# Kernel optimization log

Measured on AMD Instinct MI355X. Metric: run time of the kernel, lower is better.

The kernel has to match this reference:

```python
import jax, jax.numpy as jnp
import numpy as np

B, S, H = 32, 2048, 1024


def setup_inputs() -> dict:
    key = jax.random.key(0)
    k1, k2, k3, k4, k5, k6 = jax.random.split(key, 6)
    sc = 1.0 / np.sqrt(H)
    return {
        "dec_state": jax.random.normal(k1, (B, 1, H), dtype=jnp.float32),
        "enc_state": jax.random.normal(k2, (B, S, 2 * H), dtype=jnp.float32),
        "src_length": jax.random.randint(k3, (B,), 1, S + 1, dtype=jnp.int32),
        "W_enc": jax.random.normal(k4, (H, 2 * H), dtype=jnp.float32) * sc,
        "W_dec": jax.random.normal(k5, (H, H), dtype=jnp.float32) * sc,
        "W_energy": jax.random.normal(k6, (1, H), dtype=jnp.float32) * sc,
    }


def reference(dec_state, enc_state, src_length, W_enc, W_dec, W_energy):
    # enc: [B,S,H], dec: [B,1,H]
    enc = jnp.einsum('bse,he->bsh', enc_state, W_enc)
    dec = jnp.einsum('bod,hd->boh', dec_state, W_dec)
    # energies: [B,S] -> [B,1,S]
    energies = jnp.einsum('bsh,oh->bso', jnp.tanh(dec + enc), W_energy)[..., 0]
    mask = jnp.arange(S)[None, :] < src_length[:, None]  # [B,S]
    energies = jnp.where(mask, energies, -jnp.inf)[:, None, :]  # [B,1,S]
    alphas = jax.nn.softmax(energies, axis=-1)
    context = jnp.einsum('bos,se->boe', alphas[:, 0:1, :].squeeze(1)[:, None, :].squeeze(1)[:, None, :].squeeze(1)[:, None, :], enc_state) if False else jnp.matmul(alphas, enc_state)  # [B,1,2H]
    return context, alphas
```

## Files before the change

kernel.cpp:

```cpp
#include <hip/hip_runtime.h>
#include <hip/hip_bf16.h>
#include <stdint.h>

#define B_  32
#define S_  2048
#define H_  1024
#define K_  2048
#define M_  65536

#define BM  128
#define BN  128
#define BK  32
#define LDK 40

typedef __bf16 bf16x8 __attribute__((ext_vector_type(8)));
typedef float  f32x4  __attribute__((ext_vector_type(4)));

__device__ __forceinline__ unsigned short f2bf(float x) {
    unsigned u = __builtin_bit_cast(unsigned, x);
    u += 0x7fffu + ((u >> 16) & 1u);
    return (unsigned short)(u >> 16);
}

__device__ __forceinline__ float tanh_fast(float x) {
    float e = __expf(2.0f * x);
    return 1.0f - 2.0f / (e + 1.0f);
}

__global__ __launch_bounds__(256) void cast_k(const float* __restrict__ in,
                                              unsigned short* __restrict__ o, int n4) {
    int i = blockIdx.x * 256 + threadIdx.x;
    if (i < n4) {
        float4 v = *(const float4*)(in + (long)i * 4);
        unsigned short h0 = f2bf(v.x), h1 = f2bf(v.y), h2 = f2bf(v.z), h3 = f2bf(v.w);
        uint2 pk;
        pk.x = (unsigned)h0 | ((unsigned)h1 << 16);
        pk.y = (unsigned)h2 | ((unsigned)h3 << 16);
        *(uint2*)(o + (long)i * 4) = pk;
    }
}

__global__ __launch_bounds__(256) void dec_k(const float* __restrict__ ds,
                                             const float* __restrict__ Wd,
                                             float* __restrict__ decv) {
    const int b = blockIdx.y;
    const int w = threadIdx.x >> 6, lane = threadIdx.x & 63;
    const int h = blockIdx.x * 4 + w;
    const float* wr = Wd + (long)h * H_;
    const float* dr = ds + (long)b * H_;
    float acc = 0.f;
#pragma unroll
    for (int i = 0; i < 4; i++) {
        int idx = lane * 4 + i * 256;
        float4 a = *(const float4*)(wr + idx);
        float4 d = *(const float4*)(dr + idx);
        acc += a.x * d.x + a.y * d.y + a.z * d.z + a.w * d.w;
    }
    for (int m2 = 1; m2 < 64; m2 <<= 1) acc += __shfl_xor(acc, m2, 64);
    if (lane == 0) decv[(long)b * H_ + h] = acc;
}

__global__ __launch_bounds__(256) void gemm_energy(const float* __restrict__ A,
                                                   const unsigned short* __restrict__ Bw,
                                                   const float* __restrict__ decv,
                                                   const float* __restrict__ Weng,
                                                   float* __restrict__ pe) {
    __shared__ __align__(16) unsigned short Asm[BM * LDK];
    __shared__ __align__(16) unsigned short Bsm[BN * LDK];
    __shared__ float esum[2][BM];

    const int nb = blockIdx.x, mb = blockIdx.y;
    const int t = threadIdx.x;
    const int lane = t & 63, w = t >> 6;
    const int wm = w >> 1, wn = w & 1;
    const int r = lane & 15, g = lane >> 4;

    f32x4 acc[4][4];
#pragma unroll
    for (int mi = 0; mi < 4; mi++)
#pragma unroll
        for (int ni = 0; ni < 4; ni++)
#pragma unroll
            for (int k = 0; k < 4; k++) acc[mi][ni][k] = 0.f;

    const float* Abase = A + (long)mb * BM * K_;
    const unsigned short* Bbase = Bw + (long)nb * BN * K_;

    for (int kt = 0; kt < K_; kt += BK) {
        __syncthreads();
#pragma unroll
        for (int i = 0; i < 4; i++) {
            int f = t + 256 * i;
            int row = f >> 3, c4 = (f & 7) << 2;
            float4 v = *(const float4*)(Abase + (long)row * K_ + kt + c4);
            unsigned short h0 = f2bf(v.x), h1 = f2bf(v.y), h2 = f2bf(v.z), h3 = f2bf(v.w);
            uint2 pk;
            pk.x = (unsigned)h0 | ((unsigned)h1 << 16);
            pk.y = (unsigned)h2 | ((unsigned)h3 << 16);
            *(uint2*)&Asm[row * LDK + c4] = pk;
        }
#pragma unroll
        for (int j = 0; j < 2; j++) {
            int u = t + 256 * j;
            int row = u >> 2, c8 = (u & 3) << 3;
            uint4 v = *(const uint4*)(Bbase + (long)row * K_ + kt + c8);
            *(uint4*)&Bsm[row * LDK + c8] = v;
        }
        __syncthreads();
        bf16x8 af[4], bfr[4];
#pragma unroll
        for (int mi = 0; mi < 4; mi++)
            af[mi] = *(const bf16x8*)&Asm[(wm * 64 + mi * 16 + r) * LDK + g * 8];
#pragma unroll
        for (int ni = 0; ni < 4; ni++)
            bfr[ni] = *(const bf16x8*)&Bsm[(wn * 64 + ni * 16 + r) * LDK + g * 8];
#pragma unroll
        for (int mi = 0; mi < 4; mi++)
#pragma unroll
            for (int ni = 0; ni < 4; ni++)
                acc[mi][ni] = __builtin_amdgcn_mfma_f32_16x16x32_bf16(af[mi], bfr[ni],
                                                                     acc[mi][ni], 0, 0, 0);
    }

    const int b = mb >> 4;
    float wv[4], dv[4];
#pragma unroll
    for (int ni = 0; ni < 4; ni++) {
        int h = nb * BN + wn * 64 + ni * 16 + r;
        wv[ni] = Weng[h];
        dv[ni] = decv[b * H_ + h];
    }
    float rs[4][4];
#pragma unroll
    for (int mi = 0; mi < 4; mi++)
#pragma unroll
        for (int rr = 0; rr < 4; rr++) rs[mi][rr] = 0.f;
#pragma unroll
    for (int mi = 0; mi < 4; mi++)
#pragma unroll
        for (int ni = 0; ni < 4; ni++)
#pragma unroll
            for (int rr = 0; rr < 4; rr++)
                rs[mi][rr] += wv[ni] * tanh_fast(dv[ni] + acc[mi][ni][rr]);
#pragma unroll
    for (int m2 = 1; m2 < 16; m2 <<= 1)
#pragma unroll
        for (int mi = 0; mi < 4; mi++)
#pragma unroll
            for (int rr = 0; rr < 4; rr++)
                rs[mi][rr] += __shfl_xor(rs[mi][rr], m2, 64);
    if (r == 0) {
#pragma unroll
        for (int mi = 0; mi < 4; mi++)
#pragma unroll
            for (int rr = 0; rr < 4; rr++)
                esum[wn][wm * 64 + mi * 16 + g * 4 + rr] = rs[mi][rr];
    }
    __syncthreads();
    if (t < BM) pe[(long)nb * M_ + (long)mb * BM + t] = esum[0][t] + esum[1][t];
}

__global__ __launch_bounds__(256) void softmax_k(const float* __restrict__ pe,
                                                 const int* __restrict__ slen,
                                                 float* __restrict__ alph) {
    const int b = blockIdx.x, t = threadIdx.x;
    const int len = slen[b];
    __shared__ float sh[4];
    const float NEG = -__builtin_inff();
    float e[8];
    float mx = NEG;
#pragma unroll
    for (int i = 0; i < 8; i++) {
        int s = t + i * 256;
        float v = 0.f;
#pragma unroll
        for (int p = 0; p < 8; p++) v += pe[(long)p * M_ + b * S_ + s];
        v = (s < len) ? v : NEG;
        e[i] = v;
        mx = fmaxf(mx, v);
    }
    for (int m2 = 1; m2 < 64; m2 <<= 1) mx = fmaxf(mx, __shfl_xor(mx, m2, 64));
    if ((t & 63) == 0) sh[t >> 6] = mx;
    __syncthreads();
    mx = fmaxf(fmaxf(sh[0], sh[1]), fmaxf(sh[2], sh[3]));
    float sum = 0.f;
#pragma unroll
    for (int i = 0; i < 8; i++) {
        float x = (e[i] == NEG) ? 0.f : __expf(e[i] - mx);
        e[i] = x;
        sum += x;
    }
    for (int m2 = 1; m2 < 64; m2 <<= 1) sum += __shfl_xor(sum, m2, 64);
    __syncthreads();
    if ((t & 63) == 0) sh[t >> 6] = sum;
    __syncthreads();
    sum = sh[0] + sh[1] + sh[2] + sh[3];
    float inv = 1.0f / sum;
#pragma unroll
    for (int i = 0; i < 8; i++) alph[b * S_ + t + i * 256] = e[i] * inv;
}

__global__ __launch_bounds__(256) void context_k(const float* __restrict__ enc,
                                                 const float* __restrict__ alph,
                                                 const int* __restrict__ slen,
                                                 float* __restrict__ out) {
    const int b = blockIdx.y;
    const int x = blockIdx.x;
    const int ec = x & 1, sc = x >> 1;
    const int len = slen[b];
    const int s0 = sc * 256;
    if (s0 >= len) return;
    const int send = min(s0 + 256, len);
    __shared__ float al[256];
    const int t = threadIdx.x;
    al[t] = alph[b * S_ + s0 + t];
    __syncthreads();
    const int e0 = ec * 1024 + t * 4;
    float ax = 0.f, ay = 0.f, az = 0.f, aw = 0.f;
    const float* base = enc + ((long)b * S_ + s0) * K_ + e0;
#pragma unroll 4
    for (int s = s0; s < send; ++s) {
        float a = al[s - s0];
        float4 v = *(const float4*)base;
        ax += a * v.x; ay += a * v.y; az += a * v.z; aw += a * v.w;
        base += K_;
    }
    float* o = out + (long)b * K_ + e0;
    atomicAdd(o + 0, ax);
    atomicAdd(o + 1, ay);
    atomicAdd(o + 2, az);
    atomicAdd(o + 3, aw);
}

extern "C" void kernel_launch(void* const* d_in, const int* in_sizes, int n_in,
                              void* d_out, int out_size, void* d_ws, size_t ws_size,
                              hipStream_t stream) {
    const float* dec_state = (const float*)d_in[0];
    const float* enc_state = (const float*)d_in[1];
    const int*   src_len   = (const int*)d_in[2];
    const float* W_enc     = (const float*)d_in[3];
    const float* W_dec     = (const float*)d_in[4];
    const float* W_energy  = (const float*)d_in[5];
    float* out = (float*)d_out;

    char* ws = (char*)d_ws;
    float* decv = (float*)ws;
    float* pe   = (float*)(ws + 131072);
    unsigned short* Wenc_bf = (unsigned short*)(ws + 131072 + 2097152);
    float* alph = out + 65536;

    hipMemsetAsync(out, 0, 65536 * sizeof(float), stream);

    cast_k<<<2048, 256, 0, stream>>>(W_enc, Wenc_bf, 524288);
    dec_k<<<dim3(H_ / 4, B_), 256, 0, stream>>>(dec_state, W_dec, decv);
    gemm_energy<<<dim3(8, 512), 256, 0, stream>>>(enc_state, Wenc_bf, decv, W_energy, pe);
    softmax_k<<<B_, 256, 0, stream>>>(pe, src_len, alph);
    context_k<<<dim3(16, B_), 256, 0, stream>>>(enc_state, alph, src_len, out);
}
```

Measured before the change: 1.216 ms.

## Load B tiles via direct global-to-LDS, remap blocks per XCD, use packed bf16 convert

The B-operand tile now goes straight from global memory into shared memory with global_load_lds, which skips the register round trip. Its LDS layout loses the padding, which may bring bank conflicts on fragment reads. The grid is flattened so that the 8 N-blocks of an M row-block land on the same XCD, aiming for better L2 reuse of the fp32 A rows. The fp32-to-bf16 conversion uses the hardware packed-convert builtin when available, with the manual rounding path as a fallback.

```diff
diff --git a/kernel.cpp b/kernel.cpp
--- a/kernel.cpp
+++ b/kernel.cpp
@@ -22,6 +22,16 @@
     return (unsigned short)(u >> 16);
 }
 
+__device__ __forceinline__ unsigned pk_bf16(float x, float y) {
+#if __has_builtin(__builtin_amdgcn_cvt_pk_bf16_f32)
+    auto r = __builtin_amdgcn_cvt_pk_bf16_f32(x, y);
+    static_assert(sizeof(r) == 4, "cvt_pk_bf16 size");
+    return __builtin_bit_cast(unsigned, r);
+#else
+    return ((unsigned)f2bf(x)) | ((unsigned)f2bf(y) << 16);
+#endif
+}
+
 __device__ __forceinline__ float tanh_fast(float x) {
     float e = __expf(2.0f * x);
     return 1.0f - 2.0f / (e + 1.0f);
@@ -32,10 +42,9 @@
     int i = blockIdx.x * 256 + threadIdx.x;
     if (i < n4) {
         float4 v = *(const float4*)(in + (long)i * 4);
-        unsigned short h0 = f2bf(v.x), h1 = f2bf(v.y), h2 = f2bf(v.z), h3 = f2bf(v.w);
         uint2 pk;
-        pk.x = (unsigned)h0 | ((unsigned)h1 << 16);
-        pk.y = (unsigned)h2 | ((unsigned)h3 << 16);
+        pk.x = pk_bf16(v.x, v.y);
+        pk.y = pk_bf16(v.z, v.w);
         *(uint2*)(o + (long)i * 4) = pk;
     }
 }
@@ -66,10 +75,15 @@
                                                    const float* __restrict__ Weng,
                                                    float* __restrict__ pe) {
     __shared__ __align__(16) unsigned short Asm[BM * LDK];
-    __shared__ __align__(16) unsigned short Bsm[BN * LDK];
+    __shared__ __align__(1024) unsigned short Bsm[BN * BK];
     __shared__ float esum[2][BM];
 
-    const int nb = blockIdx.x, mb = blockIdx.y;
+    const int L = blockIdx.x;
+    const int xcd = L & 7;
+    const int slot = L >> 3;
+    const int nb = slot & 7;
+    const int mb = (slot >> 3) * 8 + xcd;
+
     const int t = threadIdx.x;
     const int lane = t & 63, w = t >> 6;
     const int wm = w >> 1, wn = w & 1;
@@ -89,22 +103,23 @@
     for (int kt = 0; kt < K_; kt += BK) {
         __syncthreads();
 #pragma unroll
+        for (int j = 0; j < 2; j++) {
+            int u = t + 256 * j;
+            int row = u >> 2, c8 = (u & 3) << 3;
+            __builtin_amdgcn_global_load_lds(
+                (const __attribute__((address_space(1))) unsigned*)(Bbase + (long)row * K_ + kt + c8),
+                (__attribute__((address_space(3))) unsigned*)&Bsm[u * 8],
+                16, 0, 0);
+        }
+#pragma unroll
         for (int i = 0; i < 4; i++) {
             int f = t + 256 * i;
             int row = f >> 3, c4 = (f & 7) << 2;
             float4 v = *(const float4*)(Abase + (long)row * K_ + kt + c4);
-            unsigned short h0 = f2bf(v.x), h1 = f2bf(v.y), h2 = f2bf(v.z), h3 = f2bf(v.w);
             uint2 pk;
-            pk.x = (unsigned)h0 | ((unsigned)h1 << 16);
-            pk.y = (unsigned)h2 | ((unsigned)h3 << 16);
+            pk.x = pk_bf16(v.x, v.y);
+            pk.y = pk_bf16(v.z, v.w);
             *(uint2*)&Asm[row * LDK + c4] = pk;
-        }
-#pragma unroll
-        for (int j = 0; j < 2; j++) {
-            int u = t + 256 * j;
-            int row = u >> 2, c8 = (u & 3) << 3;
-            uint4 v = *(const uint4*)(Bbase + (long)row * K_ + kt + c8);
-            *(uint4*)&Bsm[row * LDK + c8] = v;
         }
         __syncthreads();
         bf16x8 af[4], bfr[4];
@@ -113,7 +128,7 @@
             af[mi] = *(const bf16x8*)&Asm[(wm * 64 + mi * 16 + r) * LDK + g * 8];
 #pragma unroll
         for (int ni = 0; ni < 4; ni++)
-            bfr[ni] = *(const bf16x8*)&Bsm[(wn * 64 + ni * 16 + r) * LDK + g * 8];
+            bfr[ni] = *(const bf16x8*)&Bsm[(wn * 64 + ni * 16 + r) * BK + g * 8];
 #pragma unroll
         for (int mi = 0; mi < 4; mi++)
 #pragma unroll
@@ -253,7 +268,7 @@
 
     cast_k<<<2048, 256, 0, stream>>>(W_enc, Wenc_bf, 524288);
     dec_k<<<dim3(H_ / 4, B_), 256, 0, stream>>>(dec_state, W_dec, decv);
-    gemm_energy<<<dim3(8, 512), 256, 0, stream>>>(enc_state, Wenc_bf, decv, W_energy, pe);
+    gemm_energy<<<4096, 256, 0, stream>>>(enc_state, Wenc_bf, decv, W_energy, pe);
     softmax_k<<<B_, 256, 0, stream>>>(pe, src_len, alph);
     context_k<<<dim3(16, B_), 256, 0, stream>>>(enc_state, alph, src_len, out);
 }
```

Result: faster. 1.154 ms (-5.1%).
